# Kernel tuning notes

Hardware: AMD Instinct MI355X
Metric: run time of the kernel (lower is better)

## Reference

```python
import jax, jax.numpy as jnp
import numpy as np

N_FFT = 512
HOP = 128
WIN = 512
BATCH = 32
N_SAMPLES = 480000


def make_forward_basis():
    n_freq = N_FFT // 2 + 1  # 257
    # periodic hann window (torch.hann_window default periodic=True)
    n = np.arange(WIN, dtype=np.float32)
    window = 0.5 * (1.0 - np.cos(2.0 * np.pi * n / WIN))
    freqs = np.linspace(0.0, N_FFT // 2, n_freq, dtype=np.float32)  # [n_freq]
    t = np.arange(WIN, dtype=np.float32)
    phase = 2.0 * np.pi * freqs[:, None] * t[None, :] / N_FFT
    real = np.cos(phase) * window[None, :]
    imag = -np.sin(phase) * window[None, :]
    basis = np.concatenate([real, imag], axis=0)[:, None, :]
    return jnp.asarray(basis, dtype=jnp.float32)


def setup_inputs() -> dict:
    key = jax.random.key(0)
    x = jax.random.normal(key, (BATCH, N_SAMPLES), dtype=jnp.float32)
    return {"x": x, "forward_basis": make_forward_basis()}


def reference(x, forward_basis):
    # x: [B, T] -> [B, 1, T]
    x = x[:, None, :]
    pad = N_FFT // 2
    x_padded = jnp.pad(x, ((0, 0), (0, 0), (pad, pad)), mode="reflect")
    # single conv over concatenated real+imag basis: [B, 2*n_freq, n_frames]
    spec = jax.lax.conv_general_dilated(
        x_padded, forward_basis,
        window_strides=(HOP,), padding="VALID",
        dimension_numbers=("NCH", "OIH", "NCH"))
    n_freq = N_FFT // 2 + 1
    real_spec = spec[:, :n_freq, :]
    imag_spec = spec[:, n_freq:, :]
    return jnp.sqrt(real_spec ** 2 + imag_spec ** 2)
```

## Files before the change

kernel.cpp:

```cpp
#include <hip/hip_runtime.h>

#define NFREQ   257
#define NFRAMES 3751
#define NS      480000
#define HOP     128
#define WIN     512

#define NB      32
#define BN      128
#define NFT     30
#define STEPS   32
#define XWPITCH 272
#define XW_B    35632
#define AHALF   16384
#define WNYQ_B  2048
#define XGROUPS 2096

typedef __attribute__((ext_vector_type(8))) short short8;
typedef __attribute__((ext_vector_type(4))) float f32x4;

__device__ __forceinline__ short f2bf(float f) {
    __bf16 b = (__bf16)f;
    return __builtin_bit_cast(short, b);
}
__device__ __forceinline__ float bf2f(short s) {
    unsigned int u = ((unsigned int)(unsigned short)s) << 16;
    return __builtin_bit_cast(float, u);
}
__device__ __forceinline__ void gload_lds16(const void* g, void* l) {
    __builtin_amdgcn_global_load_lds(
        (const __attribute__((address_space(1))) void*)g,
        (__attribute__((address_space(3))) void*)l, 16, 0, 0);
}

__global__ __launch_bounds__(256)
void prep_basis4(const float* __restrict__ basis,
                 short* __restrict__ abL, short* __restrict__ wnyqG) {
    int g = blockIdx.x * 256 + threadIdx.x;
    if (g < 32768) {
        int ob   = g * 16;
        int step = ob >> 14;
        int rem  = ob & 16383;
        int pl   = rem >> 13;
        int r    = (rem >> 7) & 63;
        int s    = (rem >> 4) & 7;
        int u    = s ^ (r & 7);
        int f    = r + (u >> 2) * 64;
        int kg   = u & 3;
        int fp   = step >> 4;
        int ks32 = step & 15;
        int row  = pl * NFREQ + fp * 128 + f;
        int k0   = ks32 * 32 + kg * 8;
        const float4* p = reinterpret_cast<const float4*>(
            basis + (size_t)row * WIN + k0);
        float4 a0 = p[0], a1 = p[1];
        short8 v;
        v[0]=f2bf(a0.x); v[1]=f2bf(a0.y); v[2]=f2bf(a0.z); v[3]=f2bf(a0.w);
        v[4]=f2bf(a1.x); v[5]=f2bf(a1.y); v[6]=f2bf(a1.z); v[7]=f2bf(a1.w);
        *reinterpret_cast<short8*>(reinterpret_cast<char*>(abL) + ob) = v;
    } else if (g < 32832) {
        int j = g - 32768;
        const float4* p = reinterpret_cast<const float4*>(basis + (size_t)256 * WIN + j * 8);
        float4 a0 = p[0], a1 = p[1];
        short8 v;
        v[0]=f2bf(a0.x); v[1]=f2bf(a0.y); v[2]=f2bf(a0.z); v[3]=f2bf(a0.w);
        v[4]=f2bf(a1.x); v[5]=f2bf(a1.y); v[6]=f2bf(a1.z); v[7]=f2bf(a1.w);
        *reinterpret_cast<short8*>(wnyqG + j * 8) = v;
    }
}

__global__ __launch_bounds__(256, 2)
void stft_mfma_kernel(const float* __restrict__ x,
                      const short* __restrict__ abL,
                      const short* __restrict__ wnyqG,
                      float* __restrict__ out)
{
    __shared__ __align__(16) char smem[XW_B + 2 * AHALF + WNYQ_B];
    char* const xw   = smem;
    char* const aBuf = smem + XW_B;
    float* const wny = reinterpret_cast<float*>(smem + XW_B + 2 * AHALF);

    const int tid  = threadIdx.x;
    const int wave = tid >> 6;
    const int lane = tid & 63;
    const int lgrp = lane >> 4;
    const int l15  = lane & 15;

    const int logical = (blockIdx.x & 7) * 120 + (blockIdx.x >> 3);
    const int ft = logical % NFT;
    const int b  = logical / NFT;
    const int t0 = ft * BN;

    const char* abLc = (const char*)abL;

    #pragma unroll
    for (int i = 0; i < 4; ++i) {
        int c = wave * 4 + i;
        gload_lds16(abLc + c * 1024 + lane * 16, aBuf + c * 1024);
    }
    {
        short a0 = wnyqG[tid * 2], a1 = wnyqG[tid * 2 + 1];
        wny[tid * 2]     = bf2f(a0);
        wny[tid * 2 + 1] = bf2f(a1);
    }

    {
        const float* __restrict__ xb = x + (size_t)b * NS;
        const int sbase = t0 * 128 - 256;
        #pragma unroll
        for (int i = 0; i < 9; ++i) {
            int g = tid + i * 256;
            if (g < XGROUPS) {
                int ix = sbase + g * 8;
                short8 v;
                if (ix >= 0 && ix + 8 <= NS) {
                    const float4* p = reinterpret_cast<const float4*>(xb + ix);
                    float4 a0 = p[0], a1 = p[1];
                    v[0]=f2bf(a0.x); v[1]=f2bf(a0.y); v[2]=f2bf(a0.z); v[3]=f2bf(a0.w);
                    v[4]=f2bf(a1.x); v[5]=f2bf(a1.y); v[6]=f2bf(a1.z); v[7]=f2bf(a1.w);
                } else {
                    #pragma unroll
                    for (int q = 0; q < 8; ++q) {
                        int idx = ix + q;
                        if (idx < 0) idx = -idx;
                        if (idx >= NS + 256) { v[q] = 0; continue; }
                        if (idx >= NS) idx = 2 * NS - 2 - idx;
                        v[q] = f2bf(xb[idx]);
                    }
                }
                *reinterpret_cast<short8*>(xw + (g >> 4) * XWPITCH + (g & 15) * 16) = v;
            }
        }
    }

    f32x4 accR[2][8], accI[2][8];
    #pragma unroll
    for (int m = 0; m < 2; ++m)
        #pragma unroll
        for (int n = 0; n < 8; ++n) {
            accR[m][n] = f32x4{0.f,0.f,0.f,0.f};
            accI[m][n] = f32x4{0.f,0.f,0.f,0.f};
        }

    const int rb = (wave & 1) * 32 + l15;
    const int ub = (wave >> 1) * 4 + lgrp;

    const int nfl = wave * 32 + (lane & 31);
    const int nh  = lane >> 5;
    const int nyqXbase = (nfl + 2 * nh) * XWPITCH;
    const float* const nyqW = wny + nh * 256;
    float nacc = 0.f;

    #pragma unroll 1
    for (int s = 0; s < STEPS; ++s) {
        asm volatile("s_waitcnt vmcnt(0)" ::: "memory");
        __builtin_amdgcn_sched_barrier(0);
        __syncthreads();
        __builtin_amdgcn_sched_barrier(0);

        char* const aCur = aBuf + (s & 1) * AHALF;

        if (s + 1 < STEPS) {
            char* const aNxt = aBuf + ((s + 1) & 1) * AHALF;
            const char* sb = abLc + (size_t)(s + 1) * AHALF;
            #pragma unroll
            for (int i = 0; i < 4; ++i) {
                int c = wave * 4 + i;
                gload_lds16(sb + c * 1024 + lane * 16, aNxt + c * 1024);
            }
        }
        __builtin_amdgcn_sched_barrier(0);

        const int ks32 = s & 15;
        short8 aRv[2], aIv[2], xv[8];
        #pragma unroll
        for (int m = 0; m < 2; ++m) {
            int r   = rb + m * 16;
            int off = r * 128 + ((ub ^ (r & 7)) << 4);
            aRv[m] = *reinterpret_cast<const short8*>(aCur + off);
            aIv[m] = *reinterpret_cast<const short8*>(aCur + 8192 + off);
        }
        {
            int r8 = ks32 * 64 + lgrp * 16;
            int T  = r8 + ((r8 >> 8) << 4);
            const char* xwl = xw + l15 * XWPITCH + T;
            #pragma unroll
            for (int nt = 0; nt < 8; ++nt)
                xv[nt] = *reinterpret_cast<const short8*>(xwl + nt * (16 * XWPITCH));
        }
        #pragma unroll
        for (int m = 0; m < 2; ++m)
            #pragma unroll
            for (int nt = 0; nt < 8; ++nt) {
                accR[m][nt] = __builtin_amdgcn_mfma_f32_16x16x32_bf16(aRv[m], xv[nt], accR[m][nt], 0, 0, 0);
                accI[m][nt] = __builtin_amdgcn_mfma_f32_16x16x32_bf16(aIv[m], xv[nt], accI[m][nt], 0, 0, 0);
            }

        {
            short8 nx = *reinterpret_cast<const short8*>(
                xw + nyqXbase + (s >> 4) * XWPITCH + (s & 15) * 16);
            const float* wrow = nyqW + s * 8;
            #pragma unroll
            for (int q = 0; q < 8; ++q)
                nacc = fmaf(bf2f(nx[q]), wrow[q], nacc);
        }

        if ((s & 15) == 15) {
            const int fp = s >> 4;
            float* ob = out + (size_t)b * NFREQ * NFRAMES;
            const int fb = fp * 128 + wave * 32 + lgrp * 4;
            const int tb = t0 + l15;
            #pragma unroll
            for (int m = 0; m < 2; ++m)
                #pragma unroll
                for (int nt = 0; nt < 8; ++nt) {
                    int t = tb + nt * 16;
                    if (t < NFRAMES) {
                        #pragma unroll
                        for (int r = 0; r < 4; ++r) {
                            int f = fb + m * 16 + r;
                            float vr = accR[m][nt][r], vi = accI[m][nt][r];
                            ob[(size_t)f * NFRAMES + t] =
                                __builtin_amdgcn_sqrtf(vr * vr + vi * vi);
                        }
                    }
                    accR[m][nt] = f32x4{0.f,0.f,0.f,0.f};
                    accI[m][nt] = f32x4{0.f,0.f,0.f,0.f};
                }
        }
    }

    {
        nacc += __shfl_xor(nacc, 32);
        int t = t0 + nfl;
        if (nh == 0 && t < NFRAMES)
            out[((size_t)b * NFREQ + 256) * NFRAMES + t] = fabsf(nacc);
    }
}

extern "C" void kernel_launch(void* const* d_in, const int* in_sizes, int n_in,
                              void* d_out, int out_size, void* d_ws, size_t ws_size,
                              hipStream_t stream) {
    const float* x     = (const float*)d_in[0];
    const float* basis = (const float*)d_in[1];
    float* out = (float*)d_out;

    short* abL   = (short*)d_ws;
    short* wnyqG = abL + 262144;

    prep_basis4<<<dim3(129), 256, 0, stream>>>(basis, abL, wnyqG);
    stft_mfma_kernel<<<dim3(NFT * NB), 256, 0, stream>>>(x, abL, wnyqG, out);
}
```

Before: 80.99 us.

## Give each wave a private basis slice in LDS and drop per-step barrier

The prep kernel now lays out the bf16 basis so each wave's A-fragments sit in a contiguous private 4 KB region, in per-lane MFMA operand order. Each wave then loads and reads only its own region, so the per-step __syncthreads in the K loop is removed and a single barrier after the x-window staging remains. This targets barrier stalls and swizzled LDS addressing, but the per-wave vmcnt wait and the double-buffer reuse now depend on wave-local ordering only.

```diff
diff --git a/kernel.cpp b/kernel.cpp
--- a/kernel.cpp
+++ b/kernel.cpp
@@ -34,25 +34,22 @@
 }
 
 __global__ __launch_bounds__(256)
-void prep_basis4(const float* __restrict__ basis,
+void prep_basis7(const float* __restrict__ basis,
                  short* __restrict__ abL, short* __restrict__ wnyqG) {
     int g = blockIdx.x * 256 + threadIdx.x;
     if (g < 32768) {
         int ob   = g * 16;
         int step = ob >> 14;
-        int rem  = ob & 16383;
-        int pl   = rem >> 13;
-        int r    = (rem >> 7) & 63;
-        int s    = (rem >> 4) & 7;
-        int u    = s ^ (r & 7);
-        int f    = r + (u >> 2) * 64;
-        int kg   = u & 3;
-        int fp   = step >> 4;
-        int ks32 = step & 15;
-        int row  = pl * NFREQ + fp * 128 + f;
-        int k0   = ks32 * 32 + kg * 8;
+        int w    = (ob >> 12) & 3;
+        int pl   = (ob >> 11) & 1;
+        int m    = (ob >> 10) & 1;
+        int perm = (ob >> 4) & 63;
+        int l15  = perm >> 2;
+        int lgrp = perm & 3;
+        int fr   = (step >> 4) * 128 + w * 32 + m * 16 + l15;
+        int k0   = (step & 15) * 32 + lgrp * 8;
         const float4* p = reinterpret_cast<const float4*>(
-            basis + (size_t)row * WIN + k0);
+            basis + ((size_t)(pl * NFREQ + fr)) * WIN + k0);
         float4 a0 = p[0], a1 = p[1];
         short8 v;
         v[0]=f2bf(a0.x); v[1]=f2bf(a0.y); v[2]=f2bf(a0.z); v[3]=f2bf(a0.w);
@@ -92,12 +89,12 @@
     const int t0 = ft * BN;
 
     const char* abLc = (const char*)abL;
+    const int wBase = wave * 4096;
 
     #pragma unroll
-    for (int i = 0; i < 4; ++i) {
-        int c = wave * 4 + i;
-        gload_lds16(abLc + c * 1024 + lane * 16, aBuf + c * 1024);
-    }
+    for (int i = 0; i < 4; ++i)
+        gload_lds16(abLc + wBase + i * 1024 + lane * 16,
+                    aBuf + wBase + i * 1024);
     {
         short a0 = wnyqG[tid * 2], a1 = wnyqG[tid * 2 + 1];
         wny[tid * 2]     = bf2f(a0);
@@ -132,6 +129,7 @@
             }
         }
     }
+    __syncthreads();
 
     f32x4 accR[2][8], accI[2][8];
     #pragma unroll
@@ -142,8 +140,7 @@
             accI[m][n] = f32x4{0.f,0.f,0.f,0.f};
         }
 
-    const int rb = (wave & 1) * 32 + l15;
-    const int ub = (wave >> 1) * 4 + lgrp;
+    const int aPerm = (l15 * 4 + lgrp) * 16;
 
     const int nfl = wave * 32 + (lane & 31);
     const int nh  = lane >> 5;
@@ -155,30 +152,23 @@
     for (int s = 0; s < STEPS; ++s) {
         asm volatile("s_waitcnt vmcnt(0)" ::: "memory");
         __builtin_amdgcn_sched_barrier(0);
-        __syncthreads();
+
+        if (s + 1 < STEPS) {
+            const char* sb = abLc + (size_t)(s + 1) * AHALF + wBase;
+            char* dst = aBuf + ((s + 1) & 1) * AHALF + wBase;
+            #pragma unroll
+            for (int i = 0; i < 4; ++i)
+                gload_lds16(sb + i * 1024 + lane * 16, dst + i * 1024);
+        }
         __builtin_amdgcn_sched_barrier(0);
 
-        char* const aCur = aBuf + (s & 1) * AHALF;
-
-        if (s + 1 < STEPS) {
-            char* const aNxt = aBuf + ((s + 1) & 1) * AHALF;
-            const char* sb = abLc + (size_t)(s + 1) * AHALF;
-            #pragma unroll
-            for (int i = 0; i < 4; ++i) {
-                int c = wave * 4 + i;
-                gload_lds16(sb + c * 1024 + lane * 16, aNxt + c * 1024);
-            }
-        }
-        __builtin_amdgcn_sched_barrier(0);
-
         const int ks32 = s & 15;
+        const char* aCur = aBuf + (s & 1) * AHALF + wBase;
         short8 aRv[2], aIv[2], xv[8];
         #pragma unroll
         for (int m = 0; m < 2; ++m) {
-            int r   = rb + m * 16;
-            int off = r * 128 + ((ub ^ (r & 7)) << 4);
-            aRv[m] = *reinterpret_cast<const short8*>(aCur + off);
-            aIv[m] = *reinterpret_cast<const short8*>(aCur + 8192 + off);
+            aRv[m] = *reinterpret_cast<const short8*>(aCur + m * 1024 + aPerm);
+            aIv[m] = *reinterpret_cast<const short8*>(aCur + 2048 + m * 1024 + aPerm);
         }
         {
             int r8 = ks32 * 64 + lgrp * 16;
@@ -248,6 +238,6 @@
     short* abL   = (short*)d_ws;
     short* wnyqG = abL + 262144;
 
-    prep_basis4<<<dim3(129), 256, 0, stream>>>(basis, abL, wnyqG);
+    prep_basis7<<<dim3(129), 256, 0, stream>>>(basis, abL, wnyqG);
     stft_mfma_kernel<<<dim3(NFT * NB), 256, 0, stream>>>(x, abL, wnyqG, out);
 }
```

Result: faster. 77.73 us (-4.0%).
